# Optimization experiments

Measured on AMD Instinct MI355X. Metric: run time of the kernel, lower is better.

## Reference

```python
import jax, jax.numpy as jnp
import numpy as np

N = 50000
E = 625000
D_IN, D_HID, D_EMB, D_OUT = 256, 128, 128, 16


def glorot(key, shape):
    lim = jnp.sqrt(6.0 / (shape[0] + shape[1]))
    return jax.random.uniform(key, shape, jnp.float32, -lim, lim)


def setup_inputs() -> dict:
    key = jax.random.key(0)
    ks = jax.random.split(key, 8)
    x = jax.random.normal(ks[0], (N, D_IN), jnp.float32)
    edge_index = jax.random.randint(ks[1], (2, E), 0, N, jnp.int64)
    edge_weight = jax.random.uniform(ks[2], (E,), jnp.float32)
    return {
        "x": x,
        "edge_weight": edge_weight,
        "W1": glorot(ks[3], (D_IN, D_HID)),
        "b1": jnp.zeros((D_HID,), jnp.float32),
        "W2": glorot(ks[4], (D_HID, D_HID)),
        "b2": jnp.zeros((D_HID,), jnp.float32),
        "W3": glorot(ks[5], (D_HID, D_EMB)),
        "b3": jnp.zeros((D_EMB,), jnp.float32),
        "fc_w": glorot(ks[6], (D_EMB, D_OUT)),
        "fc_b": jnp.zeros((D_OUT,), jnp.float32),
        "edge_index": edge_index,
    }


def digcn_conv(x, edge_index, norm, W, b):
    # dense transform, then edge-weighted gather/scatter-add (SpMM)
    h = x @ W                                  # [N, d_out]
    msg = h[edge_index[0]] * norm[:, None]     # [E, d_out]
    agg = jax.ops.segment_sum(msg, edge_index[1], num_segments=N)
    return agg + b


def reference(x, edge_weight, W1, b1, W2, b2, W3, b3, fc_w, fc_b, edge_index):
    # eval mode: dropout is identity
    h = jax.nn.relu(digcn_conv(x, edge_index, edge_weight, W1, b1))
    h = jax.nn.relu(digcn_conv(h, edge_index, edge_weight, W2, b2))
    emb = digcn_conv(h, edge_index, edge_weight, W3, b3)
    y = emb @ fc_w + fc_b
    return emb, jax.nn.log_softmax(y, axis=1)
```

## Files before the change

kernel.cpp:

```cpp
#include <hip/hip_runtime.h>

#define D_IN 256
#define D_HID 128
#define NPB 512
#define BCAP 8192

typedef __bf16 bf16;
typedef bf16 bf16x8 __attribute__((ext_vector_type(8)));
typedef float f32x4 __attribute__((ext_vector_type(4)));
typedef unsigned long long u64;
typedef u64 u64x2 __attribute__((ext_vector_type(2)));

__global__ void k_prep(const float* __restrict__ W1, const float* __restrict__ W2,
                       const float* __restrict__ W3, const float* __restrict__ fcw,
                       bf16* __restrict__ B1, bf16* __restrict__ B2,
                       bf16* __restrict__ B3, float* __restrict__ fcwT,
                       int* __restrict__ gcnt, int ncnt) {
  int idx = blockIdx.x * blockDim.x + threadIdx.x;
  {
    const float* W; bf16* B; int r;
    if (idx < 32768)      { W = W1; B = B1; r = idx; }
    else if (idx < 49152) { W = W2; B = B2; r = idx - 32768; }
    else                  { W = W3; B = B3; r = idx - 49152; }
    int e = r & 7, l = (r >> 3) & 63, f = r >> 9;
    int ct = f & 7, kt = f >> 3;
    int k = kt * 32 + ((l >> 4) << 3) + e;
    int c = ct * 16 + (l & 15);
    B[r] = (bf16)W[k * 128 + c];
  }
  if (idx < 2048) {
    int c = idx >> 7, k = idx & 127;
    fcwT[idx] = fcw[k * 16 + c];
  }
  if (idx < ncnt) gcnt[idx] = 0;
}

__global__ __launch_bounds__(256) void k_bin(const int* __restrict__ src,
                                             const int* __restrict__ dst,
                                             const float* __restrict__ ew, int E,
                                             int* __restrict__ gcnt,
                                             int2* __restrict__ bins) {
  __shared__ int lcnt[128], lbase[128], lcur[128], gbase[128];
  __shared__ int stot;
  __shared__ int2 stage[2048];
  const int t = threadIdx.x;
  const int e0 = blockIdx.x * 2048;

  if (t < 128) lcnt[t] = 0;
  __syncthreads();

  int2 ent[8]; int bk[8];
  #pragma unroll
  for (int i = 0; i < 8; ++i) {
    int e = e0 + i * 256 + t;
    bool v = e < E;
    int d = v ? dst[e] : 0;
    int s = v ? src[e] : 0;
    float w = v ? ew[e] : 0.f;
    int b = d >> 9;
    bk[i] = v ? b : -1;
    ent[i] = make_int2(s | ((d & 511) << 16) | (b << 25), __float_as_int(w));
    if (v) atomicAdd(&lcnt[b], 1);
  }
  __syncthreads();

  int v = (t < 128) ? lcnt[t] : 0;
  if (t < 128) lbase[t] = v;
  __syncthreads();
  for (int off = 1; off < 128; off <<= 1) {
    int u = (t < 128 && t >= off) ? lbase[t - off] : 0;
    __syncthreads();
    if (t < 128) lbase[t] += u;
    __syncthreads();
  }
  if (t == 127) stot = lbase[127];
  if (t < 128) {
    int ex = lbase[t] - v;
    lbase[t] = ex;
    lcur[t] = ex;
    gbase[t] = (v > 0) ? atomicAdd(&gcnt[t * 16], v) : 0;
  }
  __syncthreads();

  #pragma unroll
  for (int i = 0; i < 8; ++i) {
    if (bk[i] >= 0) {
      int pos = atomicAdd(&lcur[bk[i]], 1);
      stage[pos] = ent[i];
    }
  }
  __syncthreads();

  const int tot = stot;
  for (int j = t; j < tot; j += 256) {
    int2 en = stage[j];
    int b = (en.x >> 25) & 0x7F;
    int gp = gbase[b] + (j - lbase[b]);
    if (gp < BCAP)
      bins[(size_t)b * BCAP + gp] = make_int2(en.x & 0x01FFFFFF, en.y);
  }
}

__global__ __launch_bounds__(128) void k_bsum(const int* __restrict__ gcnt, int nbk,
                                              int* __restrict__ rbase,
                                              int* __restrict__ rptr, int N) {
  __shared__ int sm[128];
  int t = threadIdx.x;
  int v = (t < nbk) ? min(gcnt[t * 16], BCAP) : 0;
  sm[t] = v; __syncthreads();
  for (int off = 1; off < 128; off <<= 1) {
    int u = (t >= off) ? sm[t - off] : 0;
    __syncthreads();
    sm[t] += u; __syncthreads();
  }
  if (t < nbk) rbase[t] = sm[t] - v;
  if (t == 127) rptr[N] = sm[127];
}

__global__ __launch_bounds__(512) void k_build(const int2* __restrict__ bins,
                                               const int* __restrict__ gcnt,
                                               const int* __restrict__ rbase,
                                               int* __restrict__ rptr,
                                               int2* __restrict__ esw, int N) {
  __shared__ int deg[512], sm[512], cur[512];
  __shared__ int cnt, base;
  const int b = blockIdx.x, t = threadIdx.x;
  const int n0 = b << 9;
  deg[t] = 0;
  if (t == 0) { cnt = min(gcnt[b * 16], BCAP); base = rbase[b]; }
  __syncthreads();
  const int2* bp = bins + (size_t)b * BCAP;
  const int c = cnt;
  for (int i = t; i < c; i += 512) atomicAdd(&deg[(bp[i].x >> 16) & 511], 1);
  __syncthreads();
  sm[t] = deg[t];
  __syncthreads();
  for (int off = 1; off < 512; off <<= 1) {
    int u = (t >= off) ? sm[t - off] : 0;
    __syncthreads();
    sm[t] += u;
    __syncthreads();
  }
  int ex = sm[t] - deg[t];
  cur[t] = ex;
  if (n0 + t < N) rptr[n0 + t] = base + ex;
  __syncthreads();
  for (int i = t; i < c; i += 512) {
    int2 en = bp[i];
    int pos = atomicAdd(&cur[(en.x >> 16) & 511], 1);
    esw[base + pos] = make_int2(en.x & 0xFFFF, en.y);
  }
}

template<int K, bool A_IS_F32>
__global__ __launch_bounds__(512) void k_gemm2(const void* __restrict__ Ain,
                                               const bf16* __restrict__ Bp,
                                               bf16* __restrict__ Hb, int N) {
  constexpr int NCH = K / 128;
  __shared__ bf16 Bs[128 * 128];
  const int t = threadIdx.x;
  const int wave = t >> 6;
  const int lane = t & 63;
  const int l16 = lane & 15;
  const int g = lane >> 4;
  const int row0 = blockIdx.x * 128 + wave * 16;
  const int arow = row0 + l16;
  const int arow_c = (arow < N) ? arow : (N - 1);

  f32x4 acc[8];
  #pragma unroll
  for (int ct = 0; ct < 8; ++ct) acc[ct] = f32x4{0.f, 0.f, 0.f, 0.f};

  for (int kc = 0; kc < NCH; ++kc) {
    if (kc) __syncthreads();
    const u64x2* src = reinterpret_cast<const u64x2*>(Bp + (size_t)kc * 128 * 128);
    u64x2* dstl = reinterpret_cast<u64x2*>(Bs);
    #pragma unroll
    for (int i = 0; i < 4; ++i) dstl[t + i * 512] = src[t + i * 512];
    __syncthreads();

    bf16x8 afr[4];
    if constexpr (A_IS_F32) {
      const float* Af = (const float*)Ain + (size_t)arow_c * K + kc * 128 + g * 8;
      #pragma unroll
      for (int kt = 0; kt < 4; ++kt) {
        f32x4 f0 = *reinterpret_cast<const f32x4*>(Af + kt * 32);
        f32x4 f1 = *reinterpret_cast<const f32x4*>(Af + kt * 32 + 4);
        bf16x8 a;
        a[0] = (bf16)f0[0]; a[1] = (bf16)f0[1]; a[2] = (bf16)f0[2]; a[3] = (bf16)f0[3];
        a[4] = (bf16)f1[0]; a[5] = (bf16)f1[1]; a[6] = (bf16)f1[2]; a[7] = (bf16)f1[3];
        afr[kt] = a;
      }
    } else {
      const bf16* Ab = (const bf16*)Ain + (size_t)arow_c * K + kc * 128 + g * 8;
      #pragma unroll
      for (int kt = 0; kt < 4; ++kt)
        afr[kt] = *reinterpret_cast<const bf16x8*>(Ab + kt * 32);
    }

    #pragma unroll
    for (int kt = 0; kt < 4; ++kt) {
      #pragma unroll
      for (int ct = 0; ct < 8; ++ct) {
        bf16x8 bfr = *reinterpret_cast<const bf16x8*>(Bs + (kt * 8 + ct) * 512 + lane * 8);
        acc[ct] = __builtin_amdgcn_mfma_f32_16x16x32_bf16(afr[kt], bfr, acc[ct], 0, 0, 0);
      }
    }
  }

  const int orow = row0 + 4 * g;
  #pragma unroll
  for (int ct = 0; ct < 8; ++ct) {
    #pragma unroll
    for (int r = 0; r < 4; ++r) {
      if (orow + r < N)
        Hb[(size_t)(orow + r) * 128 + ct * 16 + l16] = (bf16)acc[ct][r];
    }
  }
}

template<int MODE>
__global__ __launch_bounds__(256) void k_agg(const bf16* __restrict__ H,
                                             const int* __restrict__ rptr,
                                             const int2* __restrict__ esw,
                                             const float* __restrict__ bias,
                                             void* __restrict__ out, int N) {
  const int wv = threadIdx.x >> 6;
  const int lane = threadIdx.x & 63;
  const int node = blockIdx.x * 8 + wv * 2 + (lane >> 5);
  if (node >= N) return;
  const int l16 = lane & 15;
  const int slot = (lane >> 4) & 1;
  const int p1 = rptr[node + 1];
  float a[8];
  #pragma unroll
  for (int j = 0; j < 8; ++j) a[j] = 0.f;

  int p = rptr[node] + slot;
  for (; p + 2 < p1; p += 4) {
    int2 e0 = esw[p];
    int2 e1 = esw[p + 2];
    bf16x8 h0 = *reinterpret_cast<const bf16x8*>(H + (size_t)e0.x * 128 + l16 * 8);
    bf16x8 h1 = *reinterpret_cast<const bf16x8*>(H + (size_t)e1.x * 128 + l16 * 8);
    float w0 = __int_as_float(e0.y), w1 = __int_as_float(e1.y);
    #pragma unroll
    for (int j = 0; j < 8; ++j)
      a[j] += w0 * (float)h0[j] + w1 * (float)h1[j];
  }
  if (p < p1) {
    int2 e0 = esw[p];
    bf16x8 h0 = *reinterpret_cast<const bf16x8*>(H + (size_t)e0.x * 128 + l16 * 8);
    float w0 = __int_as_float(e0.y);
    #pragma unroll
    for (int j = 0; j < 8; ++j)
      a[j] += w0 * (float)h0[j];
  }
  #pragma unroll
  for (int j = 0; j < 8; ++j) a[j] += __shfl_xor(a[j], 16);

  if ((lane & 16) == 0) {
    float4 b0 = *reinterpret_cast<const float4*>(bias + l16 * 8);
    float4 b1 = *reinterpret_cast<const float4*>(bias + l16 * 8 + 4);
    a[0] += b0.x; a[1] += b0.y; a[2] += b0.z; a[3] += b0.w;
    a[4] += b1.x; a[5] += b1.y; a[6] += b1.z; a[7] += b1.w;
    if (MODE == 0) {
      bf16x8 o;
      #pragma unroll
      for (int j = 0; j < 8; ++j) o[j] = (bf16)fmaxf(a[j], 0.f);
      *reinterpret_cast<bf16x8*>((bf16*)out + (size_t)node * 128 + l16 * 8) = o;
    } else {
      f32x4 o0 = {a[0], a[1], a[2], a[3]};
      f32x4 o1 = {a[4], a[5], a[6], a[7]};
      float* op = (float*)out + (size_t)node * 128 + l16 * 8;
      *reinterpret_cast<f32x4*>(op) = o0;
      *reinterpret_cast<f32x4*>(op + 4) = o1;
    }
  }
}

__global__ __launch_bounds__(256) void k_fc_lsm(const float* __restrict__ emb,
                                                const float* __restrict__ fcwT,
                                                const float* __restrict__ fcb,
                                                float* __restrict__ out, int N) {
  __shared__ float wl[16 * 128];
  __shared__ float fb[16];
  const int t = threadIdx.x;
  {
    const float4* s4 = reinterpret_cast<const float4*>(fcwT);
    float4* d4 = reinterpret_cast<float4*>(wl);
    d4[t] = s4[t];
    d4[t + 256] = s4[t + 256];
  }
  if (t < 16) fb[t] = fcb[t];
  __syncthreads();

  const int node = blockIdx.x * 256 + t;
  if (node >= N) return;
  const float4* er = reinterpret_cast<const float4*>(emb + (size_t)node * 128);

  float acc[16];
  #pragma unroll
  for (int c = 0; c < 16; ++c) acc[c] = fb[c];

  #pragma unroll 4
  for (int k4 = 0; k4 < 32; ++k4) {
    float4 e = er[k4];
    #pragma unroll
    for (int c = 0; c < 16; ++c) {
      float4 w = reinterpret_cast<const float4*>(wl + c * 128)[k4];
      acc[c] += e.x * w.x + e.y * w.y + e.z * w.z + e.w * w.w;
    }
  }

  float m = acc[0];
  #pragma unroll
  for (int c = 1; c < 16; ++c) m = fmaxf(m, acc[c]);
  float s = 0.f;
  #pragma unroll
  for (int c = 0; c < 16; ++c) s += __expf(acc[c] - m);
  float lse = m + __logf(s);
  float* op = out + (size_t)node * 16;
  #pragma unroll
  for (int c4 = 0; c4 < 4; ++c4) {
    f32x4 o = {acc[c4 * 4] - lse, acc[c4 * 4 + 1] - lse,
               acc[c4 * 4 + 2] - lse, acc[c4 * 4 + 3] - lse};
    *reinterpret_cast<f32x4*>(op + c4 * 4) = o;
  }
}

extern "C" void kernel_launch(void* const* d_in, const int* in_sizes, int n_in,
                              void* d_out, int out_size, void* d_ws, size_t ws_size,
                              hipStream_t stream) {
  const float* x   = (const float*)d_in[0];
  const float* ew  = (const float*)d_in[1];
  const float* W1  = (const float*)d_in[2];
  const float* b1  = (const float*)d_in[3];
  const float* W2  = (const float*)d_in[4];
  const float* b2  = (const float*)d_in[5];
  const float* W3  = (const float*)d_in[6];
  const float* b3  = (const float*)d_in[7];
  const float* fcw = (const float*)d_in[8];
  const float* fcb = (const float*)d_in[9];
  const int*   ei  = (const int*)d_in[10];

  const int N = in_sizes[0] / D_IN;
  const int E = in_sizes[1];
  const int* srcI = ei;
  const int* dstI = ei + E;
  const int NBK = (N + NPB - 1) / NPB;
  const int ncnt = NBK * 16;

  char* ws = (char*)d_ws;
  size_t o = 0;
  auto take = [&](size_t b) -> char* {
    char* p = ws + o;
    o += (b + 255) & ~(size_t)255;
    return p;
  };
  bf16*  hb0  = (bf16*)take((size_t)N * 128 * 2);
  bf16*  hb1  = (bf16*)take((size_t)N * 128 * 2);
  bf16*  Bp1  = (bf16*)take((size_t)D_IN * 128 * 2);
  bf16*  Bp2  = (bf16*)take((size_t)D_HID * 128 * 2);
  bf16*  Bp3  = (bf16*)take((size_t)D_HID * 128 * 2);
  float* fcwT = (float*)take((size_t)2048 * 4);
  int*   rptr = (int*)take((size_t)(N + 1) * 4);
  int*   gcnt = (int*)take((size_t)ncnt * 4);
  int*   rbase= (int*)take((size_t)NBK * 4);
  int2*  bins = (int2*)take((size_t)NBK * BCAP * 8);
  int2*  esw  = (int2*)take((size_t)E * 8);
  (void)ws_size; (void)n_in; (void)out_size;

  k_prep<<<256, 256, 0, stream>>>(W1, W2, W3, fcw, Bp1, Bp2, Bp3, fcwT, gcnt, ncnt);

  int bb = (E + 2047) / 2048;
  k_bin<<<bb, 256, 0, stream>>>(srcI, dstI, ew, E, gcnt, bins);
  k_bsum<<<1, 128, 0, stream>>>(gcnt, NBK, rbase, rptr, N);
  k_build<<<NBK, 512, 0, stream>>>(bins, gcnt, rbase, rptr, esw, N);

  float* emb = (float*)d_out;
  float* lsm = emb + (size_t)N * 128;
  int gb2 = (N + 127) / 128;
  int ab = (N + 7) / 8;

  k_gemm2<D_IN, true><<<gb2, 512, 0, stream>>>(x, Bp1, hb0, N);
  k_agg<0><<<ab, 256, 0, stream>>>(hb0, rptr, esw, b1, hb1, N);
  k_gemm2<D_HID, false><<<gb2, 512, 0, stream>>>(hb1, Bp2, hb0, N);
  k_agg<0><<<ab, 256, 0, stream>>>(hb0, rptr, esw, b2, hb1, N);
  k_gemm2<D_HID, false><<<gb2, 512, 0, stream>>>(hb1, Bp3, hb0, N);
  k_agg<1><<<ab, 256, 0, stream>>>(hb0, rptr, esw, b3, emb, N);
  k_fc_lsm<<<(N + 255) / 256, 256, 0, stream>>>(emb, fcwT, fcb, lsm, N);
}
```

Baseline: 171.1 us.

## Restructure GEMM to per-wave column tiles reading B directly, dropping LDS staging

The dense transform kernel no longer stages the packed weight matrix in shared memory with block barriers. Each 256-thread block now covers 64 rows, and each wave computes 4 row tiles by 2 column tiles, loading its B fragments straight from global memory (likely cache-resident) and reusing them across the 4 row tiles. This removes the LDS fill, the barriers and the per-block LDS footprint. In exchange, each A row is loaded redundantly by all 4 waves, relying on cache hits, and B is fetched per wave from global memory.

After: 204.8 us. 19.7% more time.

```diff
diff --git a/kernel.cpp b/kernel.cpp
--- a/kernel.cpp
+++ b/kernel.cpp
@@ -153,68 +153,72 @@
 }
 
 template<int K, bool A_IS_F32>
-__global__ __launch_bounds__(512) void k_gemm2(const void* __restrict__ Ain,
+__global__ __launch_bounds__(256) void k_gemm4(const void* __restrict__ Ain,
                                                const bf16* __restrict__ Bp,
                                                bf16* __restrict__ Hb, int N) {
-  constexpr int NCH = K / 128;
-  __shared__ bf16 Bs[128 * 128];
+  constexpr int NKT = K / 32;
   const int t = threadIdx.x;
   const int wave = t >> 6;
   const int lane = t & 63;
   const int l16 = lane & 15;
   const int g = lane >> 4;
-  const int row0 = blockIdx.x * 128 + wave * 16;
-  const int arow = row0 + l16;
-  const int arow_c = (arow < N) ? arow : (N - 1);
-
-  f32x4 acc[8];
-  #pragma unroll
-  for (int ct = 0; ct < 8; ++ct) acc[ct] = f32x4{0.f, 0.f, 0.f, 0.f};
-
-  for (int kc = 0; kc < NCH; ++kc) {
-    if (kc) __syncthreads();
-    const u64x2* src = reinterpret_cast<const u64x2*>(Bp + (size_t)kc * 128 * 128);
-    u64x2* dstl = reinterpret_cast<u64x2*>(Bs);
-    #pragma unroll
-    for (int i = 0; i < 4; ++i) dstl[t + i * 512] = src[t + i * 512];
-    __syncthreads();
-
-    bf16x8 afr[4];
+  const int row0 = blockIdx.x * 64;
+  const int ct0 = wave * 2;
+
+  int ar[4];
+  #pragma unroll
+  for (int rt = 0; rt < 4; ++rt) {
+    int r = row0 + rt * 16 + l16;
+    ar[rt] = (r < N) ? r : (N - 1);
+  }
+
+  const bf16x8* Bv = reinterpret_cast<const bf16x8*>(Bp);
+  f32x4 acc[4][2];
+  #pragma unroll
+  for (int rt = 0; rt < 4; ++rt) {
+    acc[rt][0] = f32x4{0.f, 0.f, 0.f, 0.f};
+    acc[rt][1] = f32x4{0.f, 0.f, 0.f, 0.f};
+  }
+
+  #pragma unroll
+  for (int kt = 0; kt < NKT; ++kt) {
+    bf16x8 b0 = Bv[(size_t)(kt * 8 + ct0) * 64 + lane];
+    bf16x8 b1 = Bv[(size_t)(kt * 8 + ct0 + 1) * 64 + lane];
+    bf16x8 a[4];
     if constexpr (A_IS_F32) {
-      const float* Af = (const float*)Ain + (size_t)arow_c * K + kc * 128 + g * 8;
       #pragma unroll
-      for (int kt = 0; kt < 4; ++kt) {
-        f32x4 f0 = *reinterpret_cast<const f32x4*>(Af + kt * 32);
-        f32x4 f1 = *reinterpret_cast<const f32x4*>(Af + kt * 32 + 4);
-        bf16x8 a;
-        a[0] = (bf16)f0[0]; a[1] = (bf16)f0[1]; a[2] = (bf16)f0[2]; a[3] = (bf16)f0[3];
-        a[4] = (bf16)f1[0]; a[5] = (bf16)f1[1]; a[6] = (bf16)f1[2]; a[7] = (bf16)f1[3];
-        afr[kt] = a;
+      for (int rt = 0; rt < 4; ++rt) {
+        const float* Af = (const float*)Ain + (size_t)ar[rt] * K + kt * 32 + g * 8;
+        f32x4 f0 = *reinterpret_cast<const f32x4*>(Af);
+        f32x4 f1 = *reinterpret_cast<const f32x4*>(Af + 4);
+        bf16x8 av;
+        av[0] = (bf16)f0[0]; av[1] = (bf16)f0[1]; av[2] = (bf16)f0[2]; av[3] = (bf16)f0[3];
+        av[4] = (bf16)f1[0]; av[5] = (bf16)f1[1]; av[6] = (bf16)f1[2]; av[7] = (bf16)f1[3];
+        a[rt] = av;
       }
     } else {
-      const bf16* Ab = (const bf16*)Ain + (size_t)arow_c * K + kc * 128 + g * 8;
       #pragma unroll
-      for (int kt = 0; kt < 4; ++kt)
-        afr[kt] = *reinterpret_cast<const bf16x8*>(Ab + kt * 32);
-    }
-
-    #pragma unroll
-    for (int kt = 0; kt < 4; ++kt) {
+      for (int rt = 0; rt < 4; ++rt)
+        a[rt] = *reinterpret_cast<const bf16x8*>(
+            (const bf16*)Ain + (size_t)ar[rt] * K + kt * 32 + g * 8);
+    }
+    #pragma unroll
+    for (int rt = 0; rt < 4; ++rt) {
+      acc[rt][0] = __builtin_amdgcn_mfma_f32_16x16x32_bf16(a[rt], b0, acc[rt][0], 0, 0, 0);
+      acc[rt][1] = __builtin_amdgcn_mfma_f32_16x16x32_bf16(a[rt], b1, acc[rt][1], 0, 0, 0);
+    }
+  }
+
+  #pragma unroll
+  for (int rt = 0; rt < 4; ++rt) {
+    const int orow = row0 + rt * 16 + 4 * g;
+    #pragma unroll
+    for (int c = 0; c < 2; ++c) {
       #pragma unroll
-      for (int ct = 0; ct < 8; ++ct) {
-        bf16x8 bfr = *reinterpret_cast<const bf16x8*>(Bs + (kt * 8 + ct) * 512 + lane * 8);
-        acc[ct] = __builtin_amdgcn_mfma_f32_16x16x32_bf16(afr[kt], bfr, acc[ct], 0, 0, 0);
+      for (int r = 0; r < 4; ++r) {
+        if (orow + r < N)
+          Hb[(size_t)(orow + r) * 128 + (ct0 + c) * 16 + l16] = (bf16)acc[rt][c][r];
       }
-    }
-  }
-
-  const int orow = row0 + 4 * g;
-  #pragma unroll
-  for (int ct = 0; ct < 8; ++ct) {
-    #pragma unroll
-    for (int r = 0; r < 4; ++r) {
-      if (orow + r < N)
-        Hb[(size_t)(orow + r) * 128 + ct * 16 + l16] = (bf16)acc[ct][r];
     }
   }
 }
@@ -379,14 +383,14 @@
 
   float* emb = (float*)d_out;
   float* lsm = emb + (size_t)N * 128;
-  int gb2 = (N + 127) / 128;
+  int gb4 = (N + 63) / 64;
   int ab = (N + 7) / 8;
 
-  k_gemm2<D_IN, true><<<gb2, 512, 0, stream>>>(x, Bp1, hb0, N);
+  k_gemm4<D_IN, true><<<gb4, 256, 0, stream>>>(x, Bp1, hb0, N);
   k_agg<0><<<ab, 256, 0, stream>>>(hb0, rptr, esw, b1, hb1, N);
-  k_gemm2<D_HID, false><<<gb2, 512, 0, stream>>>(hb1, Bp2, hb0, N);
+  k_gemm4<D_HID, false><<<gb4, 256, 0, stream>>>(hb1, Bp2, hb0, N);
   k_agg<0><<<ab, 256, 0, stream>>>(hb0, rptr, esw, b2, hb1, N);
-  k_gemm2<D_HID, false><<<gb2, 512, 0, stream>>>(hb1, Bp3, hb0, N);
+  k_gemm4<D_HID, false><<<gb4, 256, 0, stream>>>(hb1, Bp3, hb0, N);
   k_agg<1><<<ab, 256, 0, stream>>>(hb0, rptr, esw, b3, emb, N);
   k_fc_lsm<<<(N + 255) / 256, 256, 0, stream>>>(emb, fcwT, fcb, lsm, N);
 }
```

## Load whole weight matrix into LDS via direct global-to-LDS loads, overlap with A loads

Applied to the files above, without the earlier changes.

The GEMM now stages the entire K×128 weight matrix into shared memory in one pass using global_load_lds, which bypasses registers. All A-fragment loads for the full K are issued before the single barrier, so A traffic overlaps the B staging. This replaces the per-128-chunk loop with its repeated barriers. Blocks shrink to 256 threads and 64 rows, doubling the grid, but LDS use grows to 64KB for K=256 and more A registers are live, which may limit occupancy.

After: 175.2 us. 2.4% more time.

```diff
diff --git a/kernel.cpp b/kernel.cpp
--- a/kernel.cpp
+++ b/kernel.cpp
@@ -8,8 +8,8 @@
 typedef __bf16 bf16;
 typedef bf16 bf16x8 __attribute__((ext_vector_type(8)));
 typedef float f32x4 __attribute__((ext_vector_type(4)));
-typedef unsigned long long u64;
-typedef u64 u64x2 __attribute__((ext_vector_type(2)));
+typedef const __attribute__((address_space(1))) unsigned gu32;
+typedef __attribute__((address_space(3))) unsigned lu32;
 
 __global__ void k_prep(const float* __restrict__ W1, const float* __restrict__ W2,
                        const float* __restrict__ W3, const float* __restrict__ fcw,
@@ -153,58 +153,65 @@
 }
 
 template<int K, bool A_IS_F32>
-__global__ __launch_bounds__(512) void k_gemm2(const void* __restrict__ Ain,
+__global__ __launch_bounds__(256) void k_gemm5(const void* __restrict__ Ain,
                                                const bf16* __restrict__ Bp,
                                                bf16* __restrict__ Hb, int N) {
-  constexpr int NCH = K / 128;
-  __shared__ bf16 Bs[128 * 128];
+  constexpr int NKT = K / 32;
+  constexpr int NST = (K * 128) / (256 * 8);
+  __shared__ bf16 Bs[K * 128];
   const int t = threadIdx.x;
   const int wave = t >> 6;
   const int lane = t & 63;
   const int l16 = lane & 15;
   const int g = lane >> 4;
-  const int row0 = blockIdx.x * 128 + wave * 16;
+  const int row0 = blockIdx.x * 64 + wave * 16;
   const int arow = row0 + l16;
   const int arow_c = (arow < N) ? arow : (N - 1);
 
+  #pragma unroll
+  for (int i = 0; i < NST; ++i) {
+    const bf16* gsrc = Bp + (size_t)(i * 256 + t) * 8;
+    bf16* ldst = Bs + (size_t)(i * 256 + (t & ~63)) * 8;
+    __builtin_amdgcn_global_load_lds((gu32*)gsrc, (lu32*)ldst, 16, 0, 0);
+  }
+
+  bf16x8 afr[NKT];
+  if constexpr (A_IS_F32) {
+    const float* Af = (const float*)Ain + (size_t)arow_c * K + g * 8;
+    f32x4 f0[NKT], f1[NKT];
+    #pragma unroll
+    for (int kt = 0; kt < NKT; ++kt) {
+      f0[kt] = *reinterpret_cast<const f32x4*>(Af + kt * 32);
+      f1[kt] = *reinterpret_cast<const f32x4*>(Af + kt * 32 + 4);
+    }
+    #pragma unroll
+    for (int kt = 0; kt < NKT; ++kt) {
+      bf16x8 a;
+      a[0] = (bf16)f0[kt][0]; a[1] = (bf16)f0[kt][1];
+      a[2] = (bf16)f0[kt][2]; a[3] = (bf16)f0[kt][3];
+      a[4] = (bf16)f1[kt][0]; a[5] = (bf16)f1[kt][1];
+      a[6] = (bf16)f1[kt][2]; a[7] = (bf16)f1[kt][3];
+      afr[kt] = a;
+    }
+  } else {
+    const bf16* Ab = (const bf16*)Ain + (size_t)arow_c * K + g * 8;
+    #pragma unroll
+    for (int kt = 0; kt < NKT; ++kt)
+      afr[kt] = *reinterpret_cast<const bf16x8*>(Ab + kt * 32);
+  }
+
+  __syncthreads();
+
   f32x4 acc[8];
   #pragma unroll
   for (int ct = 0; ct < 8; ++ct) acc[ct] = f32x4{0.f, 0.f, 0.f, 0.f};
 
-  for (int kc = 0; kc < NCH; ++kc) {
-    if (kc) __syncthreads();
-    const u64x2* src = reinterpret_cast<const u64x2*>(Bp + (size_t)kc * 128 * 128);
-    u64x2* dstl = reinterpret_cast<u64x2*>(Bs);
-    #pragma unroll
-    for (int i = 0; i < 4; ++i) dstl[t + i * 512] = src[t + i * 512];
-    __syncthreads();
-
-    bf16x8 afr[4];
-    if constexpr (A_IS_F32) {
-      const float* Af = (const float*)Ain + (size_t)arow_c * K + kc * 128 + g * 8;
-      #pragma unroll
-      for (int kt = 0; kt < 4; ++kt) {
-        f32x4 f0 = *reinterpret_cast<const f32x4*>(Af + kt * 32);
-        f32x4 f1 = *reinterpret_cast<const f32x4*>(Af + kt * 32 + 4);
-        bf16x8 a;
-        a[0] = (bf16)f0[0]; a[1] = (bf16)f0[1]; a[2] = (bf16)f0[2]; a[3] = (bf16)f0[3];
-        a[4] = (bf16)f1[0]; a[5] = (bf16)f1[1]; a[6] = (bf16)f1[2]; a[7] = (bf16)f1[3];
-        afr[kt] = a;
-      }
-    } else {
-      const bf16* Ab = (const bf16*)Ain + (size_t)arow_c * K + kc * 128 + g * 8;
-      #pragma unroll
-      for (int kt = 0; kt < 4; ++kt)
-        afr[kt] = *reinterpret_cast<const bf16x8*>(Ab + kt * 32);
-    }
-
-    #pragma unroll
-    for (int kt = 0; kt < 4; ++kt) {
-      #pragma unroll
-      for (int ct = 0; ct < 8; ++ct) {
-        bf16x8 bfr = *reinterpret_cast<const bf16x8*>(Bs + (kt * 8 + ct) * 512 + lane * 8);
-        acc[ct] = __builtin_amdgcn_mfma_f32_16x16x32_bf16(afr[kt], bfr, acc[ct], 0, 0, 0);
-      }
+  #pragma unroll
+  for (int kt = 0; kt < NKT; ++kt) {
+    #pragma unroll
+    for (int ct = 0; ct < 8; ++ct) {
+      bf16x8 b = *reinterpret_cast<const bf16x8*>(Bs + (kt * 8 + ct) * 512 + lane * 8);
+      acc[ct] = __builtin_amdgcn_mfma_f32_16x16x32_bf16(afr[kt], b, acc[ct], 0, 0, 0);
     }
   }
 
@@ -379,14 +386,14 @@
 
   float* emb = (float*)d_out;
   float* lsm = emb + (size_t)N * 128;
-  int gb2 = (N + 127) / 128;
+  int gb5 = (N + 63) / 64;
   int ab = (N + 7) / 8;
 
-  k_gemm2<D_IN, true><<<gb2, 512, 0, stream>>>(x, Bp1, hb0, N);
+  k_gemm5<D_IN, true><<<gb5, 256, 0, stream>>>(x, Bp1, hb0, N);
   k_agg<0><<<ab, 256, 0, stream>>>(hb0, rptr, esw, b1, hb1, N);
-  k_gemm2<D_HID, false><<<gb2, 512, 0, stream>>>(hb1, Bp2, hb0, N);
+  k_gemm5<D_HID, false><<<gb5, 256, 0, stream>>>(hb1, Bp2, hb0, N);
   k_agg<0><<<ab, 256, 0, stream>>>(hb0, rptr, esw, b2, hb1, N);
-  k_gemm2<D_HID, false><<<gb2, 512, 0, stream>>>(hb1, Bp3, hb0, N);
+  k_gemm5<D_HID, false><<<gb5, 256, 0, stream>>>(hb1, Bp3, hb0, N);
   k_agg<1><<<ab, 256, 0, stream>>>(hb0, rptr, esw, b3, emb, N);
   k_fc_lsm<<<(N + 255) / 256, 256, 0, stream>>>(emb, fcwT, fcb, lsm, N);
 }
```
